# Optimization experiments

Measured on AMD Instinct MI355X. Metric: run time of the kernel, lower is better.

## Reference

```python
import jax, jax.numpy as jnp
import numpy as np

B, N, DIM, K, H, R = 128, 196, 384, 16, 6, 4  # batch, tokens, channels, bases, heads, adapter ratio


def setup_inputs() -> dict:
    key = jax.random.key(0)
    ks = jax.random.split(key, 4)
    d_r = DIM // R
    return {
        "x": jax.random.normal(ks[0], (B, N, DIM), jnp.float32),
        "W1": jax.random.normal(ks[1], (DIM, d_r), jnp.float32) * 0.02,
        "b1": jnp.zeros((d_r,), jnp.float32),
        "W2": jax.random.normal(ks[2], (d_r, K * H), jnp.float32) * 0.02,
        "b2": jnp.zeros((K * H,), jnp.float32),
        "weight_bank": jax.random.normal(ks[3], (K, N, N), jnp.float32) * 0.02,
    }


def reference(x, W1, b1, W2, b2, weight_bank):
    Bsz, n, C = x.shape
    hdim = C // H
    # adapter MLP: Linear -> GELU(exact/erf, torch default) -> Linear
    hid = jax.nn.gelu(x @ W1 + b1, approximate=False)
    mix = (hid @ W2 + b2).reshape(Bsz, n, K, H)
    # mode='softmax': normalize mixing policy over the k bases
    mix = jax.nn.softmax(mix, axis=2)
    # dynamic per-sample token-mixing matrix [B, n, n, H]
    weight = jnp.einsum('bnkh,knm->bnmh', mix, weight_bank)
    # mix tokens: contract over source token index n
    xh = x.reshape(Bsz, n, H, hdim)
    out = jnp.einsum('bnhc,bnmh->bmhc', xh, weight).reshape(Bsz, n, C)
    return out
```

## Files before the change

kernel.cpp:

```cpp
#include <hip/hip_runtime.h>
#include <math.h>

#define BB  128
#define NN  196
#define CDIM 384
#define KK  16
#define HH  6
#define DR  96
#define HD  64
#define MP  208
#define NCHUNK 7
#define PLANE 6656

typedef __attribute__((ext_vector_type(8))) short bf16x8;
typedef __attribute__((ext_vector_type(4))) float f32x4;

__device__ __forceinline__ unsigned short f2bf(float f) {
    unsigned u = __float_as_uint(f);
    u += 0x7FFFu + ((u >> 16) & 1u);
    return (unsigned short)(u >> 16);
}
__device__ __forceinline__ unsigned pk2bf(float lo, float hi) {
    return (unsigned)f2bf(lo) | ((unsigned)f2bf(hi) << 16);
}

union AFrag { unsigned u[4]; bf16x8 f; };

__global__ __launch_bounds__(256) void prep_kernel(
    const float* __restrict__ W1, const float* __restrict__ W2,
    const float* __restrict__ wb,
    unsigned short* __restrict__ W1T, unsigned short* __restrict__ W2T,
    unsigned short* __restrict__ wbT)
{
    const int bid = blockIdx.x;
    const int t   = threadIdx.x;
    if (bid < DR) {
        const int c = bid;
        for (int k = t; k < CDIM; k += 256)
            W1T[(size_t)c * CDIM + k] = f2bf(W1[(size_t)k * DR + c]);
        if (t < DR)
            W2T[(size_t)c * DR + t] = f2bf(W2[(size_t)t * DR + c]);
    } else {
        const int n = bid - DR;
        const int m = t;
        if (m < MP) {
            unsigned o[8] = {0u, 0u, 0u, 0u, 0u, 0u, 0u, 0u};
            if (n < NN && m < NN) {
                #pragma unroll
                for (int j = 0; j < 8; ++j) {
                    const float a = wb[((size_t)(2 * j)     * NN + n) * NN + m];
                    const float c = wb[((size_t)(2 * j + 1) * NN + n) * NN + m];
                    o[j] = pk2bf(a, c);
                }
            }
            unsigned* dst = (unsigned*)(wbT + ((size_t)n * MP + m) * KK);
            *(uint4*)dst       = make_uint4(o[0], o[1], o[2], o[3]);
            *(uint4*)(dst + 4) = make_uint4(o[4], o[5], o[6], o[7]);
        }
    }
}

__global__ __launch_bounds__(128, 3) void adapter_kernel(
    const float* __restrict__ x,   const unsigned short* __restrict__ W1T,
    const float* __restrict__ b1,  const unsigned short* __restrict__ W2T,
    const float* __restrict__ b2,  unsigned short* __restrict__ mix_out)
{
    __shared__ unsigned short hidb[16][104];

    const int t    = threadIdx.x;
    const int wc   = t >> 6;
    const int lane = t & 63;
    const int l15  = lane & 15;
    const int lq   = lane >> 4;
    const int row0 = blockIdx.x * 16;

    f32x4 acc[3];
    #pragma unroll
    for (int ct = 0; ct < 3; ++ct) {
        const float bj = b1[wc * 48 + ct * 16 + l15];
        acc[ct] = (f32x4){bj, bj, bj, bj};
    }
    const float* xrow = x + (size_t)(row0 + l15) * CDIM;
    for (int kc = 0; kc < CDIM; kc += 32) {
        const float4 u = *(const float4*)(xrow + kc + 8 * lq);
        const float4 v = *(const float4*)(xrow + kc + 8 * lq + 4);
        AFrag af;
        af.u[0] = pk2bf(u.x, u.y); af.u[1] = pk2bf(u.z, u.w);
        af.u[2] = pk2bf(v.x, v.y); af.u[3] = pk2bf(v.z, v.w);
        #pragma unroll
        for (int ct = 0; ct < 3; ++ct) {
            const bf16x8 bf = *(const bf16x8*)(W1T + (size_t)(wc * 48 + ct * 16 + l15) * CDIM + kc + 8 * lq);
            acc[ct] = __builtin_amdgcn_mfma_f32_16x16x32_bf16(af.f, bf, acc[ct], 0, 0, 0);
        }
    }
    #pragma unroll
    for (int ct = 0; ct < 3; ++ct)
        #pragma unroll
        for (int r = 0; r < 4; ++r) {
            const float vv = acc[ct][r];
            hidb[lq * 4 + r][wc * 48 + ct * 16 + l15] =
                f2bf(0.5f * vv * (1.0f + erff(vv * 0.70710678118654752f)));
        }
    __syncthreads();

    f32x4 acc2[3];
    #pragma unroll
    for (int ct = 0; ct < 3; ++ct) {
        const float bj = b2[wc * 48 + ct * 16 + l15];
        acc2[ct] = (f32x4){bj, bj, bj, bj};
    }
    #pragma unroll
    for (int kc = 0; kc < DR; kc += 32) {
        const bf16x8 af = *(const bf16x8*)&hidb[l15][kc + 8 * lq];
        #pragma unroll
        for (int ct = 0; ct < 3; ++ct) {
            const bf16x8 bf = *(const bf16x8*)(W2T + (size_t)(wc * 48 + ct * 16 + l15) * DR + kc + 8 * lq);
            acc2[ct] = __builtin_amdgcn_mfma_f32_16x16x32_bf16(af, bf, acc2[ct], 0, 0, 0);
        }
    }
    __syncthreads();

    #pragma unroll
    for (int ct = 0; ct < 3; ++ct)
        #pragma unroll
        for (int r = 0; r < 4; ++r)
            hidb[lq * 4 + r][wc * 48 + ct * 16 + l15] = f2bf(acc2[ct][r]);
    __syncthreads();

    if (t < 96) {
        const int r = t / 6, h = t % 6;
        float lg[KK];
        float mx = -1e30f;
        #pragma unroll
        for (int k = 0; k < KK; ++k) {
            lg[k] = __uint_as_float((unsigned)hidb[r][6 * k + h] << 16);
            mx = fmaxf(mx, lg[k]);
        }
        float s = 0.f;
        #pragma unroll
        for (int k = 0; k < KK; ++k) { lg[k] = __expf(lg[k] - mx); s += lg[k]; }
        const float inv = 1.0f / s;
        unsigned o[8];
        #pragma unroll
        for (int jj = 0; jj < 8; ++jj)
            o[jj] = pk2bf(lg[2 * jj] * inv, lg[2 * jj + 1] * inv);
        unsigned* op = (unsigned*)(mix_out + ((size_t)(row0 + r) * HH + h) * KK);
        *(uint4*)op       = make_uint4(o[0], o[1], o[2], o[3]);
        *(uint4*)(op + 4) = make_uint4(o[4], o[5], o[6], o[7]);
    }
}

__global__ __launch_bounds__(256, 3) void aform_kernel(
    const unsigned short* __restrict__ mixb,
    const unsigned short* __restrict__ wbT,
    unsigned short* __restrict__ A)
{
    const int t    = threadIdx.x;
    const int w    = t >> 6;
    const int lane = t & 63;
    const int l15  = lane & 15;
    const int lq   = lane >> 4;
    const int b    = blockIdx.x & 127;
    const int nc   = blockIdx.x >> 7;

    const bf16x8 z8 = {0, 0, 0, 0, 0, 0, 0, 0};
    const f32x4  cz = {0.f, 0.f, 0.f, 0.f};
    const size_t bc6 = ((size_t)b * NCHUNK + nc) * HH;

    for (int i = 0; i < 8; ++i) {
        const int nl = 4 * i + w;
        const int n  = nc * 32 + nl;
        bf16x8 af = z8;
        if (n < NN && l15 < HH && lq < 2)
            af = *(const bf16x8*)(mixb + (((size_t)b * NN + n) * HH + l15) * KK + 8 * lq);
        f32x4 c[13];
        #pragma unroll
        for (int mt = 0; mt < 13; ++mt) {
            bf16x8 bf = z8;
            if (lq < 2)
                bf = *(const bf16x8*)(wbT + ((size_t)n * MP + mt * 16 + l15) * KK + 8 * lq);
            c[mt] = __builtin_amdgcn_mfma_f32_16x16x32_bf16(af, bf, cz, 0, 0, 0);
        }
        if (lq < 2) {
            unsigned short* p0 = A + (bc6 + (size_t)(lq * 4)) * PLANE + (size_t)nl * MP + l15;
            #pragma unroll
            for (int mt = 0; mt < 13; ++mt) {
                p0[mt * 16]         = f2bf(c[mt][0]);
                p0[mt * 16 + PLANE] = f2bf(c[mt][1]);
            }
            if (lq == 0) {
                #pragma unroll
                for (int mt = 0; mt < 13; ++mt) {
                    p0[mt * 16 + 2 * PLANE] = f2bf(c[mt][2]);
                    p0[mt * 16 + 3 * PLANE] = f2bf(c[mt][3]);
                }
            }
        }
    }
}

__global__ __launch_bounds__(192, 3) void mix_gemm_kernel(
    const float* __restrict__ x, const unsigned short* __restrict__ Ab,
    float* __restrict__ out)
{
    __shared__ unsigned short xT[192][40];
    __shared__ unsigned short As[3][32][68];

    const int t    = threadIdx.x;
    const int bid  = blockIdx.x;
    const int b    = bid & 127;
    const int sub  = bid >> 7;
    const int q    = sub >> 1;
    const int hp   = sub & 1;
    const int m0   = q * 52;
    const int qvalid = (q == 3) ? 40 : 52;
    const int lw   = t >> 6;
    const int hbase = hp * 3;
    const int lane = t & 63;
    const int l15  = lane & 15;
    const int lq   = lane >> 4;
    const int c0   = hp * 192;

    const f32x4 cz = {0.f, 0.f, 0.f, 0.f};
    f32x4 acc[4][4];
    #pragma unroll
    for (int mt = 0; mt < 4; ++mt)
        #pragma unroll
        for (int ct = 0; ct < 4; ++ct) acc[mt][ct] = cz;

    for (int nc = 0; nc < NCHUNK; ++nc) {
        const int n0 = nc * 32;
        __syncthreads();

        unsigned long long av[8];
        const size_t bc6 = ((size_t)b * NCHUNK + nc) * HH + hbase;
        #pragma unroll
        for (int i = 0; i < 8; ++i) {
            const int P = t + 192 * i;
            const int row = P >> 4, p = P & 15;
            const int hl = row >> 5, n = row & 31;
            av[i] = *(const unsigned long long*)(
                Ab + (bc6 + hl) * PLANE + (size_t)n * MP + m0 + 4 * p);
        }

        #pragma unroll
        for (int it = 0; it < 4; ++it) {
            const int task = t + 192 * it;
            const int p  = task & 15;
            const int cq = task >> 4;
            const int n  = n0 + 2 * p;
            float4 va = make_float4(0.f, 0.f, 0.f, 0.f);
            float4 vb = make_float4(0.f, 0.f, 0.f, 0.f);
            if (n < NN)     va = *(const float4*)(x + ((size_t)b * NN + n) * CDIM + c0 + 4 * cq);
            if (n + 1 < NN) vb = *(const float4*)(x + ((size_t)b * NN + n + 1) * CDIM + c0 + 4 * cq);
            *(unsigned*)&xT[4 * cq + 0][2 * p] = pk2bf(va.x, vb.x);
            *(unsigned*)&xT[4 * cq + 1][2 * p] = pk2bf(va.y, vb.y);
            *(unsigned*)&xT[4 * cq + 2][2 * p] = pk2bf(va.z, vb.z);
            *(unsigned*)&xT[4 * cq + 3][2 * p] = pk2bf(va.w, vb.w);
        }

        #pragma unroll
        for (int i = 0; i < 8; ++i) {
            const int P = t + 192 * i;
            const int row = P >> 4, p = P & 15;
            *(unsigned long long*)&As[row >> 5][row & 31][4 * p] = av[i];
        }
        __syncthreads();

        bf16x8 afr[4], bfr[4];
        #pragma unroll
        for (int mt = 0; mt < 4; ++mt) {
            union { unsigned short s[8]; bf16x8 v; } u;
            #pragma unroll
            for (int j = 0; j < 8; ++j)
                u.s[j] = As[lw][8 * lq + j][mt * 16 + l15];
            afr[mt] = u.v;
        }
        #pragma unroll
        for (int ct = 0; ct < 4; ++ct)
            bfr[ct] = *(const bf16x8*)&xT[lw * 64 + ct * 16 + l15][8 * lq];
        #pragma unroll
        for (int mt = 0; mt < 4; ++mt)
            #pragma unroll
            for (int ct = 0; ct < 4; ++ct)
                acc[mt][ct] = __builtin_amdgcn_mfma_f32_16x16x32_bf16(
                    afr[mt], bfr[ct], acc[mt][ct], 0, 0, 0);
    }

    const int h = hbase + lw;
    #pragma unroll
    for (int mt = 0; mt < 4; ++mt) {
        #pragma unroll
        for (int r = 0; r < 4; ++r) {
            const int ms = mt * 16 + lq * 4 + r;
            if (ms < qvalid) {
                float* op = out + ((size_t)b * NN + m0 + ms) * CDIM + h * HD + l15;
                #pragma unroll
                for (int ct = 0; ct < 4; ++ct)
                    op[ct * 16] = acc[mt][ct][r];
            }
        }
    }
}

__global__ __launch_bounds__(192, 3) void mix_mfma_fb_kernel(
    const float* __restrict__ x,  const unsigned short* __restrict__ mixb,
    const unsigned short* __restrict__ wbT, float* __restrict__ out)
{
    __shared__ unsigned short xT[192][40];
    __shared__ unsigned short Asb[3][64][40];

    const int t    = threadIdx.x;
    const int bid  = blockIdx.x;
    const int b    = bid & 127;
    const int sub  = bid >> 7;
    const int q    = sub >> 1;
    const int hp   = sub & 1;
    const int m0   = q * 52;
    const int qvalid = (q == 3) ? 40 : 52;
    const int lw   = t >> 6;
    const int hbase = hp * 3;
    const int lane = t & 63;
    const int l15  = lane & 15;
    const int lq   = lane >> 4;
    const int c0   = hp * 192;

    const bf16x8 z8 = {0, 0, 0, 0, 0, 0, 0, 0};
    const f32x4  cz = {0.f, 0.f, 0.f, 0.f};

    f32x4 acc[4][4];
    #pragma unroll
    for (int mt = 0; mt < 4; ++mt)
        #pragma unroll
        for (int ct = 0; ct < 4; ++ct) acc[mt][ct] = cz;

    for (int nc = 0; nc < 7; ++nc) {
        const int n0 = nc * 32;
        __syncthreads();

        #pragma unroll
        for (int it = 0; it < 4; ++it) {
            const int task = t + 192 * it;
            const int p  = task & 15;
            const int cq = task >> 4;
            const int n  = n0 + 2 * p;
            float4 va = make_float4(0.f, 0.f, 0.f, 0.f);
            float4 vb = make_float4(0.f, 0.f, 0.f, 0.f);
            if (n < NN)     va = *(const float4*)(x + ((size_t)b * NN + n) * CDIM + c0 + 4 * cq);
            if (n + 1 < NN) vb = *(const float4*)(x + ((size_t)b * NN + n + 1) * CDIM + c0 + 4 * cq);
            *(unsigned*)&xT[4 * cq + 0][2 * p] = pk2bf(va.x, vb.x);
            *(unsigned*)&xT[4 * cq + 1][2 * p] = pk2bf(va.y, vb.y);
            *(unsigned*)&xT[4 * cq + 2][2 * p] = pk2bf(va.z, vb.z);
            *(unsigned*)&xT[4 * cq + 3][2 * p] = pk2bf(va.w, vb.w);
        }

        for (int nl = lw; nl < 32; nl += 3) {
            const int n = n0 + nl;
            if (n < NN) {
                bf16x8 af = z8;
                if (l15 < HH && lq < 2)
                    af = *(const bf16x8*)(mixb + (((size_t)b * NN + n) * HH + l15) * KK + 8 * lq);
                #pragma unroll
                for (int mt = 0; mt < 4; ++mt) {
                    const int m = m0 + mt * 16 + l15;
                    bf16x8 bf = z8;
                    if (lq < 2 && m < NN)
                        bf = *(const bf16x8*)(wbT + ((size_t)n * MP + m) * KK + 8 * lq);
                    const f32x4 c = __builtin_amdgcn_mfma_f32_16x16x32_bf16(af, bf, cz, 0, 0, 0);
                    #pragma unroll
                    for (int r = 0; r < 4; ++r) {
                        const int hh = lq * 4 + r;
                        if (hh >= hbase && hh < hbase + 3)
                            Asb[hh - hbase][mt * 16 + l15][nl] = f2bf(c[r]);
                    }
                }
            } else {
                #pragma unroll
                for (int mt = 0; mt < 4; ++mt)
                    #pragma unroll
                    for (int r = 0; r < 4; ++r) {
                        const int hh = lq * 4 + r;
                        if (hh >= hbase && hh < hbase + 3)
                            Asb[hh - hbase][mt * 16 + l15][nl] = 0;
                    }
            }
        }
        __syncthreads();

        bf16x8 afr[4], bfr[4];
        #pragma unroll
        for (int mt = 0; mt < 4; ++mt)
            afr[mt] = *(const bf16x8*)&Asb[lw][mt * 16 + l15][8 * lq];
        #pragma unroll
        for (int ct = 0; ct < 4; ++ct)
            bfr[ct] = *(const bf16x8*)&xT[lw * 64 + ct * 16 + l15][8 * lq];
        #pragma unroll
        for (int mt = 0; mt < 4; ++mt)
            #pragma unroll
            for (int ct = 0; ct < 4; ++ct)
                acc[mt][ct] = __builtin_amdgcn_mfma_f32_16x16x32_bf16(
                    afr[mt], bfr[ct], acc[mt][ct], 0, 0, 0);
    }

    const int h = hbase + lw;
    #pragma unroll
    for (int mt = 0; mt < 4; ++mt) {
        #pragma unroll
        for (int r = 0; r < 4; ++r) {
            const int ms = mt * 16 + lq * 4 + r;
            if (ms < qvalid) {
                float* op = out + ((size_t)b * NN + m0 + ms) * CDIM + h * HD + l15;
                #pragma unroll
                for (int ct = 0; ct < 4; ++ct)
                    op[ct * 16] = acc[mt][ct][r];
            }
        }
    }
}

extern "C" void kernel_launch(void* const* d_in, const int* in_sizes, int n_in,
                              void* d_out, int out_size, void* d_ws, size_t ws_size,
                              hipStream_t stream) {
    (void)in_sizes; (void)n_in; (void)out_size;
    const float* x  = (const float*)d_in[0];
    const float* W1 = (const float*)d_in[1];
    const float* b1 = (const float*)d_in[2];
    const float* W2 = (const float*)d_in[3];
    const float* b2 = (const float*)d_in[4];
    const float* wb = (const float*)d_in[5];
    float* out = (float*)d_out;

    const size_t MIXB_OFF = 0;
    const size_t W1T_OFF  = 4816896;
    const size_t W2T_OFF  = 4890624;
    const size_t WBT_OFF  = 4909056;
    const size_t A_OFF    = 6400000;
    const size_t NEED     = A_OFF + 71565312ull + 1024ull;

    unsigned short* mixbuf = (unsigned short*)((char*)d_ws + MIXB_OFF);
    unsigned short* w1t    = (unsigned short*)((char*)d_ws + W1T_OFF);
    unsigned short* w2t    = (unsigned short*)((char*)d_ws + W2T_OFF);
    unsigned short* wbt    = (unsigned short*)((char*)d_ws + WBT_OFF);

    prep_kernel<<<DR + 224, 256, 0, stream>>>(W1, W2, wb, w1t, w2t, wbt);
    adapter_kernel<<<(BB * NN) / 16, 128, 0, stream>>>(x, w1t, b1, w2t, b2, mixbuf);

    if (ws_size >= NEED) {
        unsigned short* Ab = (unsigned short*)((char*)d_ws + A_OFF);
        aform_kernel<<<BB * NCHUNK, 256, 0, stream>>>(mixbuf, wbt, Ab);
        mix_gemm_kernel<<<8 * BB, 192, 0, stream>>>(x, Ab, out);
    } else {
        mix_mfma_fb_kernel<<<8 * BB, 192, 0, stream>>>(x, mixbuf, wbt, out);
    }
}
```

Baseline: 199.7 us.

## Fuse adapter MLP/softmax into A-forming kernel and prefetch next A chunk

The adapter MLP, GELU and softmax now run inside the kernel that builds the per-sample mixing matrix, one block per batch and 32-token chunk. The softmax weights stay in shared memory instead of going through a global mix buffer, and one kernel launch goes away. The token-mixing GEMM also loads the next chunk of A into registers while the current chunk is consumed, overlapping global loads with MFMA work. The costs are a larger fused kernel with more shared memory, rows padded past 196 that do masked work, and higher register pressure from prefetching.

```diff
diff --git a/kernel.cpp b/kernel.cpp
--- a/kernel.cpp
+++ b/kernel.cpp
@@ -60,108 +60,107 @@
     }
 }
 
-__global__ __launch_bounds__(128, 3) void adapter_kernel(
-    const float* __restrict__ x,   const unsigned short* __restrict__ W1T,
-    const float* __restrict__ b1,  const unsigned short* __restrict__ W2T,
-    const float* __restrict__ b2,  unsigned short* __restrict__ mix_out)
-{
-    __shared__ unsigned short hidb[16][104];
-
-    const int t    = threadIdx.x;
-    const int wc   = t >> 6;
-    const int lane = t & 63;
-    const int l15  = lane & 15;
-    const int lq   = lane >> 4;
-    const int row0 = blockIdx.x * 16;
-
-    f32x4 acc[3];
-    #pragma unroll
-    for (int ct = 0; ct < 3; ++ct) {
-        const float bj = b1[wc * 48 + ct * 16 + l15];
-        acc[ct] = (f32x4){bj, bj, bj, bj};
-    }
-    const float* xrow = x + (size_t)(row0 + l15) * CDIM;
-    for (int kc = 0; kc < CDIM; kc += 32) {
-        const float4 u = *(const float4*)(xrow + kc + 8 * lq);
-        const float4 v = *(const float4*)(xrow + kc + 8 * lq + 4);
-        AFrag af;
-        af.u[0] = pk2bf(u.x, u.y); af.u[1] = pk2bf(u.z, u.w);
-        af.u[2] = pk2bf(v.x, v.y); af.u[3] = pk2bf(v.z, v.w);
-        #pragma unroll
-        for (int ct = 0; ct < 3; ++ct) {
-            const bf16x8 bf = *(const bf16x8*)(W1T + (size_t)(wc * 48 + ct * 16 + l15) * CDIM + kc + 8 * lq);
-            acc[ct] = __builtin_amdgcn_mfma_f32_16x16x32_bf16(af.f, bf, acc[ct], 0, 0, 0);
-        }
-    }
-    #pragma unroll
-    for (int ct = 0; ct < 3; ++ct)
-        #pragma unroll
-        for (int r = 0; r < 4; ++r) {
-            const float vv = acc[ct][r];
-            hidb[lq * 4 + r][wc * 48 + ct * 16 + l15] =
-                f2bf(0.5f * vv * (1.0f + erff(vv * 0.70710678118654752f)));
-        }
-    __syncthreads();
-
-    f32x4 acc2[3];
-    #pragma unroll
-    for (int ct = 0; ct < 3; ++ct) {
-        const float bj = b2[wc * 48 + ct * 16 + l15];
-        acc2[ct] = (f32x4){bj, bj, bj, bj};
-    }
-    #pragma unroll
-    for (int kc = 0; kc < DR; kc += 32) {
-        const bf16x8 af = *(const bf16x8*)&hidb[l15][kc + 8 * lq];
-        #pragma unroll
-        for (int ct = 0; ct < 3; ++ct) {
-            const bf16x8 bf = *(const bf16x8*)(W2T + (size_t)(wc * 48 + ct * 16 + l15) * DR + kc + 8 * lq);
-            acc2[ct] = __builtin_amdgcn_mfma_f32_16x16x32_bf16(af, bf, acc2[ct], 0, 0, 0);
-        }
-    }
-    __syncthreads();
-
-    #pragma unroll
-    for (int ct = 0; ct < 3; ++ct)
-        #pragma unroll
-        for (int r = 0; r < 4; ++r)
-            hidb[lq * 4 + r][wc * 48 + ct * 16 + l15] = f2bf(acc2[ct][r]);
-    __syncthreads();
-
-    if (t < 96) {
-        const int r = t / 6, h = t % 6;
-        float lg[KK];
-        float mx = -1e30f;
-        #pragma unroll
-        for (int k = 0; k < KK; ++k) {
-            lg[k] = __uint_as_float((unsigned)hidb[r][6 * k + h] << 16);
-            mx = fmaxf(mx, lg[k]);
-        }
-        float s = 0.f;
-        #pragma unroll
-        for (int k = 0; k < KK; ++k) { lg[k] = __expf(lg[k] - mx); s += lg[k]; }
-        const float inv = 1.0f / s;
-        unsigned o[8];
-        #pragma unroll
-        for (int jj = 0; jj < 8; ++jj)
-            o[jj] = pk2bf(lg[2 * jj] * inv, lg[2 * jj + 1] * inv);
-        unsigned* op = (unsigned*)(mix_out + ((size_t)(row0 + r) * HH + h) * KK);
-        *(uint4*)op       = make_uint4(o[0], o[1], o[2], o[3]);
-        *(uint4*)(op + 4) = make_uint4(o[4], o[5], o[6], o[7]);
-    }
-}
-
-__global__ __launch_bounds__(256, 3) void aform_kernel(
-    const unsigned short* __restrict__ mixb,
-    const unsigned short* __restrict__ wbT,
+__global__ __launch_bounds__(256, 3) void mixa_kernel(
+    const float* __restrict__ x,  const unsigned short* __restrict__ W1T,
+    const float* __restrict__ b1, const unsigned short* __restrict__ W2T,
+    const float* __restrict__ b2, const unsigned short* __restrict__ wbT,
     unsigned short* __restrict__ A)
 {
+    __shared__ unsigned short hidb[32][104];
+    __shared__ unsigned short msc[32][96];
+
     const int t    = threadIdx.x;
     const int w    = t >> 6;
+    const int wm   = w & 1;
+    const int wc   = w >> 1;
     const int lane = t & 63;
     const int l15  = lane & 15;
     const int lq   = lane >> 4;
     const int b    = blockIdx.x & 127;
     const int nc   = blockIdx.x >> 7;
+    const int n0   = nc * 32;
+
+    f32x4 acc[3];
+    #pragma unroll
+    for (int ct = 0; ct < 3; ++ct) {
+        const float bj = b1[wc * 48 + ct * 16 + l15];
+        acc[ct] = (f32x4){bj, bj, bj, bj};
+    }
+    const int nrow = n0 + wm * 16 + l15;
+    const bool rv  = (nrow < NN);
+    const float* xrow = x + ((size_t)b * NN + nrow) * CDIM;
+    for (int kc = 0; kc < CDIM; kc += 32) {
+        float4 u = make_float4(0.f, 0.f, 0.f, 0.f);
+        float4 v = make_float4(0.f, 0.f, 0.f, 0.f);
+        if (rv) {
+            u = *(const float4*)(xrow + kc + 8 * lq);
+            v = *(const float4*)(xrow + kc + 8 * lq + 4);
+        }
+        AFrag af;
+        af.u[0] = pk2bf(u.x, u.y); af.u[1] = pk2bf(u.z, u.w);
+        af.u[2] = pk2bf(v.x, v.y); af.u[3] = pk2bf(v.z, v.w);
+        #pragma unroll
+        for (int ct = 0; ct < 3; ++ct) {
+            const bf16x8 bf = *(const bf16x8*)(W1T + (size_t)(wc * 48 + ct * 16 + l15) * CDIM + kc + 8 * lq);
+            acc[ct] = __builtin_amdgcn_mfma_f32_16x16x32_bf16(af.f, bf, acc[ct], 0, 0, 0);
+        }
+    }
+    #pragma unroll
+    for (int ct = 0; ct < 3; ++ct)
+        #pragma unroll
+        for (int r = 0; r < 4; ++r) {
+            const float vv = acc[ct][r];
+            hidb[wm * 16 + lq * 4 + r][wc * 48 + ct * 16 + l15] =
+                f2bf(0.5f * vv * (1.0f + erff(vv * 0.70710678118654752f)));
+        }
+    __syncthreads();
+
+    f32x4 acc2[3];
+    #pragma unroll
+    for (int ct = 0; ct < 3; ++ct) {
+        const float bj = b2[wc * 48 + ct * 16 + l15];
+        acc2[ct] = (f32x4){bj, bj, bj, bj};
+    }
+    #pragma unroll
+    for (int kc = 0; kc < DR; kc += 32) {
+        const bf16x8 af = *(const bf16x8*)&hidb[wm * 16 + l15][kc + 8 * lq];
+        #pragma unroll
+        for (int ct = 0; ct < 3; ++ct) {
+            const bf16x8 bf = *(const bf16x8*)(W2T + (size_t)(wc * 48 + ct * 16 + l15) * DR + kc + 8 * lq);
+            acc2[ct] = __builtin_amdgcn_mfma_f32_16x16x32_bf16(af, bf, acc2[ct], 0, 0, 0);
+        }
+    }
+    __syncthreads();
+
+    #pragma unroll
+    for (int ct = 0; ct < 3; ++ct)
+        #pragma unroll
+        for (int r = 0; r < 4; ++r)
+            hidb[wm * 16 + lq * 4 + r][wc * 48 + ct * 16 + l15] = f2bf(acc2[ct][r]);
+    __syncthreads();
+
+    if (t < 192) {
+        const int r = t / 6, h = t - r * 6;
+        float lg[KK];
+        float mx = -1e30f;
+        #pragma unroll
+        for (int k = 0; k < KK; ++k) {
+            lg[k] = __uint_as_float((unsigned)hidb[r][6 * k + h] << 16);
+            mx = fmaxf(mx, lg[k]);
+        }
+        float s = 0.f;
+        #pragma unroll
+        for (int k = 0; k < KK; ++k) { lg[k] = __expf(lg[k] - mx); s += lg[k]; }
+        const float inv = 1.0f / s;
+        unsigned o[8];
+        #pragma unroll
+        for (int jj = 0; jj < 8; ++jj)
+            o[jj] = pk2bf(lg[2 * jj] * inv, lg[2 * jj + 1] * inv);
+        unsigned* op = (unsigned*)&msc[r][16 * h];
+        *(uint4*)op       = make_uint4(o[0], o[1], o[2], o[3]);
+        *(uint4*)(op + 4) = make_uint4(o[4], o[5], o[6], o[7]);
+    }
+    __syncthreads();
 
     const bf16x8 z8 = {0, 0, 0, 0, 0, 0, 0, 0};
     const f32x4  cz = {0.f, 0.f, 0.f, 0.f};
@@ -169,10 +168,10 @@
 
     for (int i = 0; i < 8; ++i) {
         const int nl = 4 * i + w;
-        const int n  = nc * 32 + nl;
+        const int n  = n0 + nl;
         bf16x8 af = z8;
-        if (n < NN && l15 < HH && lq < 2)
-            af = *(const bf16x8*)(mixb + (((size_t)b * NN + n) * HH + l15) * KK + 8 * lq);
+        if (l15 < HH && lq < 2)
+            af = *(const bf16x8*)&msc[nl][l15 * 16 + 8 * lq];
         f32x4 c[13];
         #pragma unroll
         for (int mt = 0; mt < 13; ++mt) {
@@ -228,19 +227,28 @@
         #pragma unroll
         for (int ct = 0; ct < 4; ++ct) acc[mt][ct] = cz;
 
-    for (int nc = 0; nc < NCHUNK; ++nc) {
-        const int n0 = nc * 32;
-        __syncthreads();
-
-        unsigned long long av[8];
-        const size_t bc6 = ((size_t)b * NCHUNK + nc) * HH + hbase;
+    unsigned long long av[8];
+
+    {
+        const size_t bc6 = (size_t)b * NCHUNK * HH + hbase;
         #pragma unroll
         for (int i = 0; i < 8; ++i) {
             const int P = t + 192 * i;
             const int row = P >> 4, p = P & 15;
-            const int hl = row >> 5, n = row & 31;
             av[i] = *(const unsigned long long*)(
-                Ab + (bc6 + hl) * PLANE + (size_t)n * MP + m0 + 4 * p);
+                Ab + (bc6 + (size_t)(row >> 5)) * PLANE + (size_t)(row & 31) * MP + m0 + 4 * p);
+        }
+    }
+
+    for (int nc = 0; nc < NCHUNK; ++nc) {
+        const int n0 = nc * 32;
+        if (nc) __syncthreads();
+
+        #pragma unroll
+        for (int i = 0; i < 8; ++i) {
+            const int P = t + 192 * i;
+            const int row = P >> 4, p = P & 15;
+            *(unsigned long long*)&As[row >> 5][row & 31][4 * p] = av[i];
         }
 
         #pragma unroll
@@ -258,14 +266,18 @@
             *(unsigned*)&xT[4 * cq + 2][2 * p] = pk2bf(va.z, vb.z);
             *(unsigned*)&xT[4 * cq + 3][2 * p] = pk2bf(va.w, vb.w);
         }
-
-        #pragma unroll
-        for (int i = 0; i < 8; ++i) {
-            const int P = t + 192 * i;
-            const int row = P >> 4, p = P & 15;
-            *(unsigned long long*)&As[row >> 5][row & 31][4 * p] = av[i];
-        }
         __syncthreads();
+
+        if (nc + 1 < NCHUNK) {
+            const size_t bc6 = ((size_t)b * NCHUNK + nc + 1) * HH + hbase;
+            #pragma unroll
+            for (int i = 0; i < 8; ++i) {
+                const int P = t + 192 * i;
+                const int row = P >> 4, p = P & 15;
+                av[i] = *(const unsigned long long*)(
+                    Ab + (bc6 + (size_t)(row >> 5)) * PLANE + (size_t)(row & 31) * MP + m0 + 4 * p);
+            }
+        }
 
         bf16x8 afr[4], bfr[4];
         #pragma unroll
@@ -300,6 +312,96 @@
                     op[ct * 16] = acc[mt][ct][r];
             }
         }
+    }
+}
+
+__global__ __launch_bounds__(128, 3) void adapter_kernel(
+    const float* __restrict__ x,   const unsigned short* __restrict__ W1T,
+    const float* __restrict__ b1,  const unsigned short* __restrict__ W2T,
+    const float* __restrict__ b2,  unsigned short* __restrict__ mix_out)
+{
+    __shared__ unsigned short hidb[16][104];
+
+    const int t    = threadIdx.x;
+    const int wc   = t >> 6;
+    const int lane = t & 63;
+    const int l15  = lane & 15;
+    const int lq   = lane >> 4;
+    const int row0 = blockIdx.x * 16;
+
+    f32x4 acc[3];
+    #pragma unroll
+    for (int ct = 0; ct < 3; ++ct) {
+        const float bj = b1[wc * 48 + ct * 16 + l15];
+        acc[ct] = (f32x4){bj, bj, bj, bj};
+    }
+    const float* xrow = x + (size_t)(row0 + l15) * CDIM;
+    for (int kc = 0; kc < CDIM; kc += 32) {
+        const float4 u = *(const float4*)(xrow + kc + 8 * lq);
+        const float4 v = *(const float4*)(xrow + kc + 8 * lq + 4);
+        AFrag af;
+        af.u[0] = pk2bf(u.x, u.y); af.u[1] = pk2bf(u.z, u.w);
+        af.u[2] = pk2bf(v.x, v.y); af.u[3] = pk2bf(v.z, v.w);
+        #pragma unroll
+        for (int ct = 0; ct < 3; ++ct) {
+            const bf16x8 bf = *(const bf16x8*)(W1T + (size_t)(wc * 48 + ct * 16 + l15) * CDIM + kc + 8 * lq);
+            acc[ct] = __builtin_amdgcn_mfma_f32_16x16x32_bf16(af.f, bf, acc[ct], 0, 0, 0);
+        }
+    }
+    #pragma unroll
+    for (int ct = 0; ct < 3; ++ct)
+        #pragma unroll
+        for (int r = 0; r < 4; ++r) {
+            const float vv = acc[ct][r];
+            hidb[lq * 4 + r][wc * 48 + ct * 16 + l15] =
+                f2bf(0.5f * vv * (1.0f + erff(vv * 0.70710678118654752f)));
+        }
+    __syncthreads();
+
+    f32x4 acc2[3];
+    #pragma unroll
+    for (int ct = 0; ct < 3; ++ct) {
+        const float bj = b2[wc * 48 + ct * 16 + l15];
+        acc2[ct] = (f32x4){bj, bj, bj, bj};
+    }
+    #pragma unroll
+    for (int kc = 0; kc < DR; kc += 32) {
+        const bf16x8 af = *(const bf16x8*)&hidb[l15][kc + 8 * lq];
+        #pragma unroll
+        for (int ct = 0; ct < 3; ++ct) {
+            const bf16x8 bf = *(const bf16x8*)(W2T + (size_t)(wc * 48 + ct * 16 + l15) * DR + kc + 8 * lq);
+            acc2[ct] = __builtin_amdgcn_mfma_f32_16x16x32_bf16(af, bf, acc2[ct], 0, 0, 0);
+        }
+    }
+    __syncthreads();
+
+    #pragma unroll
+    for (int ct = 0; ct < 3; ++ct)
+        #pragma unroll
+        for (int r = 0; r < 4; ++r)
+            hidb[lq * 4 + r][wc * 48 + ct * 16 + l15] = f2bf(acc2[ct][r]);
+    __syncthreads();
+
+    if (t < 96) {
+        const int r = t / 6, h = t % 6;
+        float lg[KK];
+        float mx = -1e30f;
+        #pragma unroll
+        for (int k = 0; k < KK; ++k) {
+            lg[k] = __uint_as_float((unsigned)hidb[r][6 * k + h] << 16);
+            mx = fmaxf(mx, lg[k]);
+        }
+        float s = 0.f;
+        #pragma unroll
+        for (int k = 0; k < KK; ++k) { lg[k] = __expf(lg[k] - mx); s += lg[k]; }
+        const float inv = 1.0f / s;
+        unsigned o[8];
+        #pragma unroll
+        for (int jj = 0; jj < 8; ++jj)
+            o[jj] = pk2bf(lg[2 * jj] * inv, lg[2 * jj + 1] * inv);
+        unsigned* op = (unsigned*)(mix_out + ((size_t)(row0 + r) * HH + h) * KK);
+        *(uint4*)op       = make_uint4(o[0], o[1], o[2], o[3]);
+        *(uint4*)(op + 4) = make_uint4(o[4], o[5], o[6], o[7]);
     }
 }
 
@@ -430,26 +532,25 @@
     const float* wb = (const float*)d_in[5];
     float* out = (float*)d_out;
 
-    const size_t MIXB_OFF = 0;
-    const size_t W1T_OFF  = 4816896;
-    const size_t W2T_OFF  = 4890624;
-    const size_t WBT_OFF  = 4909056;
-    const size_t A_OFF    = 6400000;
+    const size_t W1T_OFF  = 0;
+    const size_t W2T_OFF  = 73728;
+    const size_t WBT_OFF  = 92160;
+    const size_t A_OFF    = 1583104;
     const size_t NEED     = A_OFF + 71565312ull + 1024ull;
 
-    unsigned short* mixbuf = (unsigned short*)((char*)d_ws + MIXB_OFF);
-    unsigned short* w1t    = (unsigned short*)((char*)d_ws + W1T_OFF);
-    unsigned short* w2t    = (unsigned short*)((char*)d_ws + W2T_OFF);
-    unsigned short* wbt    = (unsigned short*)((char*)d_ws + WBT_OFF);
+    unsigned short* w1t = (unsigned short*)((char*)d_ws + W1T_OFF);
+    unsigned short* w2t = (unsigned short*)((char*)d_ws + W2T_OFF);
+    unsigned short* wbt = (unsigned short*)((char*)d_ws + WBT_OFF);
 
     prep_kernel<<<DR + 224, 256, 0, stream>>>(W1, W2, wb, w1t, w2t, wbt);
-    adapter_kernel<<<(BB * NN) / 16, 128, 0, stream>>>(x, w1t, b1, w2t, b2, mixbuf);
 
     if (ws_size >= NEED) {
         unsigned short* Ab = (unsigned short*)((char*)d_ws + A_OFF);
-        aform_kernel<<<BB * NCHUNK, 256, 0, stream>>>(mixbuf, wbt, Ab);
+        mixa_kernel<<<BB * NCHUNK, 256, 0, stream>>>(x, w1t, b1, w2t, b2, wbt, Ab);
         mix_gemm_kernel<<<8 * BB, 192, 0, stream>>>(x, Ab, out);
     } else {
+        unsigned short* mixbuf = (unsigned short*)((char*)d_ws + A_OFF);
+        adapter_kernel<<<(BB * NN) / 16, 128, 0, stream>>>(x, w1t, b1, w2t, b2, mixbuf);
         mix_mfma_fb_kernel<<<8 * BB, 192, 0, stream>>>(x, mixbuf, wbt, out);
     }
 }
```

New measurement: 191.1 us. -4.3%, faster.
